# Performance work log

Measured on AMD Instinct MI355X. Metric: run time of the kernel, lower is better.

## Reference

```python
import math
import jax, jax.numpy as jnp
import numpy as np

NUM_HEADS = 32
NUM_KV_HEADS = 8
HEAD_DIM = 128
ROPE_THETA = 10000.0


def rotate_half(x):
    x1, x2 = jnp.split(x, 2, axis=-1)
    return jnp.concatenate((-x2, x1), axis=-1)


def rope_cos_sin(seq_len, dim, dtype):
    pos = jnp.arange(seq_len, dtype=jnp.float32)[:, None]            # [S,1]
    freqs = jnp.exp(-jnp.arange(0, dim, 2, dtype=jnp.float32) * (math.log(ROPE_THETA) / dim))
    ang = pos * freqs                                                # [S,D/2]
    cos = jnp.concatenate([jnp.cos(ang), jnp.cos(ang)], axis=-1)     # [S,D]
    sin = jnp.concatenate([jnp.sin(ang), jnp.sin(ang)], axis=-1)
    # broadcast over heads: [S,1,D]
    return cos[:, None, :].astype(dtype), sin[:, None, :].astype(dtype)


def setup_inputs() -> dict:
    key = jax.random.key(0)
    k1, k2, k3, k4, k5 = jax.random.split(key, 5)
    B, S, Hd = 1, 2048, 4096
    kv_dim = NUM_KV_HEADS * HEAD_DIM
    s = 0.02
    return {
        "hidden_states": jax.random.normal(k1, (B, S, Hd), jnp.float32),
        "Wq": jax.random.normal(k2, (Hd, Hd), jnp.float32) * s,
        "Wk": jax.random.normal(k3, (kv_dim, Hd), jnp.float32) * s,
        "Wv": jax.random.normal(k4, (kv_dim, Hd), jnp.float32) * s,
        "Wo": jax.random.normal(k5, (Hd, Hd), jnp.float32) * s,
    }


def reference(hidden_states, Wq, Wk, Wv, Wo):
    B, S, _ = hidden_states.shape
    H, KV, D = NUM_HEADS, NUM_KV_HEADS, HEAD_DIM
    groups = H // KV

    q = jnp.einsum('bsh,oh->bso', hidden_states, Wq).reshape(B, S, H, D)
    k = jnp.einsum('bsh,oh->bso', hidden_states, Wk).reshape(B, S, KV, D)
    v = jnp.einsum('bsh,oh->bso', hidden_states, Wv).reshape(B, S, KV, D)

    # GQA: repeat_interleave along head dim
    k = jnp.repeat(k, groups, axis=2)   # [B,S,H,D]
    v = jnp.repeat(v, groups, axis=2)

    cos, sin = rope_cos_sin(S, D, hidden_states.dtype)  # [S,1,D]
    q = q * cos + rotate_half(q) * sin
    k = k * cos + rotate_half(k) * sin

    q = q.transpose(0, 2, 1, 3)  # [B,H,S,D]
    k = k.transpose(0, 2, 1, 3)
    v = v.transpose(0, 2, 1, 3)

    scores = jnp.einsum('bhqd,bhkd->bhqk', q, k) / math.sqrt(D)
    causal = jnp.tril(jnp.ones((S, S), dtype=bool))
    scores = jnp.where(causal, scores, jnp.asarray(-1e9, scores.dtype))
    attn = jax.nn.softmax(scores, axis=-1)

    out = jnp.einsum('bhqk,bhkd->bqhd', attn, v).reshape(B, S, H * D)
    return jnp.einsum('bso,ho->bsh', out, Wo)
```

## Files before the change

kernel.cpp:

```cpp
#include <hip/hip_runtime.h>

#define S_LEN 2048
#define HD    4096
#define NH    32
#define NKV   8
#define DH    128
#define NQKV  6144
#define QKV_STRIDE_B (NQKV * 2)

typedef __bf16 bf16_t;
typedef __bf16 bf16x8 __attribute__((ext_vector_type(8)));
typedef float  f32x4  __attribute__((ext_vector_type(4)));
typedef unsigned short ushort8v __attribute__((ext_vector_type(8)));

__device__ inline unsigned short f2bf_bits(float f) {
  unsigned int u = __builtin_bit_cast(unsigned int, f);
  unsigned int r = (u + 0x7FFFu + ((u >> 16) & 1u)) >> 16;
  return (unsigned short)r;
}
__device__ inline bf16_t f2bf(float f) {
  return __builtin_bit_cast(bf16_t, f2bf_bits(f));
}
__device__ inline float bf2f(bf16_t b) {
  unsigned int u = ((unsigned int)__builtin_bit_cast(unsigned short, b)) << 16;
  return __builtin_bit_cast(float, u);
}

__device__ inline void load_lds16(const void* g, void* l) {
  __builtin_amdgcn_global_load_lds(
      (__attribute__((address_space(1))) unsigned int*)(void*)g,
      (__attribute__((address_space(3))) unsigned int*)l, 16, 0, 0);
}

__device__ inline void store_out(float* p, float v)  { *p = v; }
__device__ inline void store_out(bf16_t* p, float v) { *p = f2bf(v); }

__global__ void cvt_all_kernel(const float* __restrict__ s0, const float* __restrict__ s1,
                               const float* __restrict__ s2, const float* __restrict__ s3,
                               const float* __restrict__ s4,
                               long n0, long n1, long n2, long n3,
                               long total, bf16_t* __restrict__ dst) {
  long stride = (long)gridDim.x * blockDim.x;
  for (long i = (long)blockIdx.x * blockDim.x + threadIdx.x; i < total; i += stride) {
    const float* src;
    long rel = i;
    if (rel < n0) src = s0;
    else {
      rel -= n0;
      if (rel < n1) src = s1;
      else {
        rel -= n1;
        if (rel < n2) src = s2;
        else {
          rel -= n2;
          if (rel < n3) src = s3;
          else { rel -= n3; src = s4; }
        }
      }
    }
    float4 v0 = reinterpret_cast<const float4*>(src)[rel * 2];
    float4 v1 = reinterpret_cast<const float4*>(src)[rel * 2 + 1];
    ushort8v o;
    o[0] = f2bf_bits(v0.x); o[1] = f2bf_bits(v0.y);
    o[2] = f2bf_bits(v0.z); o[3] = f2bf_bits(v0.w);
    o[4] = f2bf_bits(v1.x); o[5] = f2bf_bits(v1.y);
    o[6] = f2bf_bits(v1.z); o[7] = f2bf_bits(v1.w);
    reinterpret_cast<ushort8v*>(dst)[i] = o;
  }
}

template <typename OutT>
__global__ __launch_bounds__(256)
void gemm_db32_kernel(const bf16_t* __restrict__ A, const bf16_t* __restrict__ B,
                      OutT* __restrict__ C, int M, int N, int K, int nbx) {
  __shared__ __align__(16) bf16_t lA[2][128 * 32];
  __shared__ __align__(16) bf16_t lB[2][128 * 32];
  const int t = threadIdx.x;
  const int lane = t & 63, wave = t >> 6;

  const int nwg = gridDim.x;
  const int orig = blockIdx.x;
  const int xcd = orig & 7;
  const int qq = nwg >> 3, rr = nwg & 7;
  const int base = (xcd < rr) ? xcd * (qq + 1) : rr * (qq + 1) + (xcd - rr) * qq;
  const int wgid = base + (orig >> 3);
  const int row0 = (wgid / nbx) * 128, col0 = (wgid % nbx) * 128;

  const int wm = (wave >> 1) * 64, wn = (wave & 1) * 64;

  const int rA = wave * 32 + (lane >> 2);
  const int cA = (lane & 3) * 8;
  const char* Asrc0 = (const char*)(A + (size_t)(row0 + rA) * K + cA);
  const char* Asrc1 = (const char*)(A + (size_t)(row0 + rA + 16) * K + cA);
  const char* Bsrc0 = (const char*)(B + (size_t)(col0 + rA) * K + cA);
  const char* Bsrc1 = (const char*)(B + (size_t)(col0 + rA + 16) * K + cA);

  const int fr = lane & 15, fq = lane >> 4;
  f32x4 acc[4][4] = {};

  auto stage = [&](int b, int k0) {
    const size_t kb = (size_t)k0 * 2;
    char* lAd = (char*)lA[b] + wave * 2048;
    char* lBd = (char*)lB[b] + wave * 2048;
    load_lds16(Asrc0 + kb, lAd);
    load_lds16(Asrc1 + kb, lAd + 1024);
    load_lds16(Bsrc0 + kb, lBd);
    load_lds16(Bsrc1 + kb, lBd + 1024);
  };

  stage(0, 0);
  int b = 0;
  for (int k0 = 0; k0 < K; k0 += 32) {
    __syncthreads();
    if (k0 + 32 < K) stage(b ^ 1, k0 + 32);

    bf16x8 af[4], bfv[4];
#pragma unroll
    for (int mi = 0; mi < 4; mi++)
      af[mi] = *reinterpret_cast<const bf16x8*>(&lA[b][(wm + mi * 16 + fr) * 32 + fq * 8]);
#pragma unroll
    for (int ni = 0; ni < 4; ni++)
      bfv[ni] = *reinterpret_cast<const bf16x8*>(&lB[b][(wn + ni * 16 + fr) * 32 + fq * 8]);
    __builtin_amdgcn_s_setprio(1);
#pragma unroll
    for (int mi = 0; mi < 4; mi++)
#pragma unroll
      for (int ni = 0; ni < 4; ni++)
        acc[mi][ni] = __builtin_amdgcn_mfma_f32_16x16x32_bf16(af[mi], bfv[ni], acc[mi][ni], 0, 0, 0);
    __builtin_amdgcn_s_setprio(0);
    b ^= 1;
  }

#pragma unroll
  for (int mi = 0; mi < 4; mi++) {
#pragma unroll
    for (int r = 0; r < 4; r++) {
      int row = row0 + wm + mi * 16 + fq * 4 + r;
      OutT* Cp = C + (size_t)row * N + col0 + wn + fr;
#pragma unroll
      for (int ni = 0; ni < 4; ni++) store_out(Cp + ni * 16, acc[mi][ni][r]);
    }
  }
}

template <typename OutT>
__global__ __launch_bounds__(256)
void gemm_db32_m64_kernel(const bf16_t* __restrict__ A, const bf16_t* __restrict__ B,
                          OutT* __restrict__ C, int M, int N, int K, int nbx) {
  __shared__ __align__(16) bf16_t lA[2][64 * 32];
  __shared__ __align__(16) bf16_t lB[2][128 * 32];
  const int t = threadIdx.x;
  const int lane = t & 63, wave = t >> 6;

  const int nwg = gridDim.x;
  const int orig = blockIdx.x;
  const int xcd = orig & 7;
  const int qq = nwg >> 3, rr = nwg & 7;
  const int base = (xcd < rr) ? xcd * (qq + 1) : rr * (qq + 1) + (xcd - rr) * qq;
  const int wgid = base + (orig >> 3);
  const int row0 = (wgid / nbx) * 64, col0 = (wgid % nbx) * 128;

  const int wm = (wave >> 1) * 32, wn = (wave & 1) * 64;

  const int rA64 = wave * 16 + (lane >> 2);
  const int cA = (lane & 3) * 8;
  const char* Asrc0 = (const char*)(A + (size_t)(row0 + rA64) * K + cA);
  const int rB = wave * 32 + (lane >> 2);
  const char* Bsrc0 = (const char*)(B + (size_t)(col0 + rB) * K + cA);
  const char* Bsrc1 = (const char*)(B + (size_t)(col0 + rB + 16) * K + cA);

  const int fr = lane & 15, fq = lane >> 4;
  f32x4 acc[2][4] = {};

  auto stage = [&](int b, int k0) {
    const size_t kb = (size_t)k0 * 2;
    char* lAd = (char*)lA[b] + wave * 1024;
    char* lBd = (char*)lB[b] + wave * 2048;
    load_lds16(Asrc0 + kb, lAd);
    load_lds16(Bsrc0 + kb, lBd);
    load_lds16(Bsrc1 + kb, lBd + 1024);
  };

  stage(0, 0);
  int b = 0;
  for (int k0 = 0; k0 < K; k0 += 32) {
    __syncthreads();
    if (k0 + 32 < K) stage(b ^ 1, k0 + 32);

    bf16x8 af[2], bfv[4];
#pragma unroll
    for (int mi = 0; mi < 2; mi++)
      af[mi] = *reinterpret_cast<const bf16x8*>(&lA[b][(wm + mi * 16 + fr) * 32 + fq * 8]);
#pragma unroll
    for (int ni = 0; ni < 4; ni++)
      bfv[ni] = *reinterpret_cast<const bf16x8*>(&lB[b][(wn + ni * 16 + fr) * 32 + fq * 8]);
    __builtin_amdgcn_s_setprio(1);
#pragma unroll
    for (int mi = 0; mi < 2; mi++)
#pragma unroll
      for (int ni = 0; ni < 4; ni++)
        acc[mi][ni] = __builtin_amdgcn_mfma_f32_16x16x32_bf16(af[mi], bfv[ni], acc[mi][ni], 0, 0, 0);
    __builtin_amdgcn_s_setprio(0);
    b ^= 1;
  }

#pragma unroll
  for (int mi = 0; mi < 2; mi++) {
#pragma unroll
    for (int r = 0; r < 4; r++) {
      int row = row0 + wm + mi * 16 + fq * 4 + r;
      OutT* Cp = C + (size_t)row * N + col0 + wn + fr;
#pragma unroll
      for (int ni = 0; ni < 4; ni++) store_out(Cp + ni * 16, acc[mi][ni][r]);
    }
  }
}

__global__ void rope_all_kernel(bf16_t* __restrict__ qkv, float qscale) {
  int idx = blockIdx.x * blockDim.x + threadIdx.x;
  int i = idx & 63;
  int hh = (idx >> 6) % (NH + NKV);
  int s = idx / (64 * (NH + NKV));
  const float NEG_LOG1E4_64 = -0.14391156f;
  float freq = __expf((float)i * NEG_LOG1E4_64);
  float ang = (float)s * freq;
  float sn, cs;
  __sincosf(ang, &sn, &cs);
  const int colbase = (hh < NH) ? hh * DH : HD + (hh - NH) * DH;
  const float scale = (hh < NH) ? qscale : 1.0f;
  bf16_t* p = qkv + (size_t)s * NQKV + colbase;
  float x1 = bf2f(p[i]);
  float x2 = bf2f(p[i + 64]);
  p[i]      = f2bf((x1 * cs - x2 * sn) * scale);
  p[i + 64] = f2bf((x2 * cs + x1 * sn) * scale);
}

__global__ void transpose_kernel(const bf16_t* __restrict__ in, bf16_t* __restrict__ out,
                                 int R, int C, int in_rstride) {
  __shared__ bf16_t tile[64][65];
  int c0 = blockIdx.x * 64, r0 = blockIdx.y * 64;
  int t = threadIdx.x;
#pragma unroll
  for (int i = 0; i < 16; i++) {
    int idx = t + i * 256;
    int r = idx >> 6, c = idx & 63;
    tile[r][c] = in[(size_t)(r0 + r) * in_rstride + c0 + c];
  }
  __syncthreads();
#pragma unroll
  for (int i = 0; i < 16; i++) {
    int idx = t + i * 256;
    int r = idx >> 6, c = idx & 63;
    out[(size_t)(c0 + r) * R + r0 + c] = tile[c][r];
  }
}

__global__ __launch_bounds__(256)
void attn_kernel(const bf16_t* __restrict__ Qkv, const bf16_t* __restrict__ Vt,
                 bf16_t* __restrict__ O) {
  __shared__ __align__(16) char lK[2][64 * 256];
  __shared__ __align__(16) char lV[2][64 * 256];
  __shared__ __align__(16) bf16_t lP[4][16 * 72];

  const int t = threadIdx.x, lane = t & 63, wave = t >> 6;
  const int h = blockIdx.y, kvh = h >> 2;
  const int pid = blockIdx.x;
  const int fr = lane & 15, fq = lane >> 4;

  const int gc = wave * 4 + (lane >> 4);
  const int sS = (lane & 15) ^ (gc & 15);
  const char* KsrcB = (const char*)(Qkv + HD + (size_t)kvh * DH) +
                      (size_t)gc * QKV_STRIDE_B + sS * 16;
  const int dVc = gc * 2 + (sS >> 3);
  const char* VsrcB = (const char*)Vt + (size_t)kvh * DH * S_LEN * 2 +
                      (size_t)dVc * 4096 + (sS & 7) * 16;
  char* dKw = (char*)lK[0] + wave * 1024;
  char* dVw = (char*)lV[0] + wave * 1024;

  auto stage = [&](int buf, int kv0) {
    char* dk = dKw + buf * (64 * 256);
    char* dv = dVw + buf * (64 * 256);
    const char* ks = KsrcB + (size_t)kv0 * QKV_STRIDE_B;
    const char* vs = VsrcB + (size_t)kv0 * 2;
#pragma unroll
    for (int i = 0; i < 4; i++) {
      load_lds16(ks + i * (16 * QKV_STRIDE_B), dk + i * 4096);
      load_lds16(vs + i * (size_t)(32 * 4096), dv + i * 4096);
    }
  };

  stage(0, 0);
  int buf = 0;

  for (int pass = 0; pass < 2; pass++) {
    const int qb = pass ? pid : (31 - pid);
    const int q0 = qb * 64 + wave * 16;

    bf16x8 qf[4];
    const bf16_t* Qp = Qkv + (size_t)(q0 + fr) * NQKV + h * DH + fq * 8;
#pragma unroll
    for (int kt = 0; kt < 4; kt++)
      qf[kt] = *reinterpret_cast<const bf16x8*>(Qp + kt * 32);

    f32x4 o_acc[8] = {};
    float m_run[4] = {-1e30f, -1e30f, -1e30f, -1e30f};
    float l_run[4] = {0.f, 0.f, 0.f, 0.f};

    for (int tt = 0; tt <= qb; tt++) {
      __syncthreads();
      if (tt < qb)            stage(buf ^ 1, (tt + 1) * 64);
      else if (pass == 0)     stage(buf ^ 1, 0);

      const char* cK = lK[buf];
      const char* cV = lV[buf];
      const bool diag = (tt == qb);

      f32x4 s_acc[4] = {};
      __builtin_amdgcn_s_setprio(1);
#pragma unroll
      for (int nt = 0; nt < 4; nt++) {
        const char* rowp = cK + (nt * 16 + fr) * 256;
#pragma unroll
        for (int kt = 0; kt < 4; kt++) {
          const bf16x8 kf = *reinterpret_cast<const bf16x8*>(
              rowp + (((kt * 4 + fq) ^ fr) << 4));
          s_acc[nt] = __builtin_amdgcn_mfma_f32_16x16x32_bf16(qf[kt], kf, s_acc[nt], 0, 0, 0);
        }
      }
      __builtin_amdgcn_s_setprio(0);

      float pmax[4];
#pragma unroll
      for (int r = 0; r < 4; r++) {
        if (diag) {
          const int qrel = wave * 16 + fq * 4 + r;
#pragma unroll
          for (int nt = 0; nt < 4; nt++)
            if (nt * 16 + fr > qrel) s_acc[nt][r] = -1e30f;
        }
        float mr = fmaxf(fmaxf(s_acc[0][r], s_acc[1][r]), fmaxf(s_acc[2][r], s_acc[3][r]));
#pragma unroll
        for (int off = 1; off < 16; off <<= 1) mr = fmaxf(mr, __shfl_xor(mr, off, 16));
        pmax[r] = mr;
      }
      bool nb = (pmax[0] > m_run[0] + 8.f) || (pmax[1] > m_run[1] + 8.f) ||
                (pmax[2] > m_run[2] + 8.f) || (pmax[3] > m_run[3] + 8.f);
      if (__any(nb)) {
#pragma unroll
        for (int r = 0; r < 4; r++) {
          float mnew = fmaxf(m_run[r], pmax[r]);
          float alpha = __expf(m_run[r] - mnew);
#pragma unroll
          for (int ni = 0; ni < 8; ni++) o_acc[ni][r] *= alpha;
          l_run[r] *= alpha;
          m_run[r] = mnew;
        }
      }
      bf16_t* lPw = lP[wave];
#pragma unroll
      for (int r = 0; r < 4; r++) {
        float p0 = __expf(s_acc[0][r] - m_run[r]);
        float p1 = __expf(s_acc[1][r] - m_run[r]);
        float p2 = __expf(s_acc[2][r] - m_run[r]);
        float p3 = __expf(s_acc[3][r] - m_run[r]);
        float sr = (p0 + p1) + (p2 + p3);
#pragma unroll
        for (int off = 1; off < 16; off <<= 1) sr += __shfl_xor(sr, off, 16);
        l_run[r] += sr;
        const int row = fq * 4 + r;
        lPw[row * 72 + fr]      = f2bf(p0);
        lPw[row * 72 + 16 + fr] = f2bf(p1);
        lPw[row * 72 + 32 + fr] = f2bf(p2);
        lPw[row * 72 + 48 + fr] = f2bf(p3);
      }

#pragma unroll
      for (int kk = 0; kk < 2; kk++) {
        const bf16x8 pf = *reinterpret_cast<const bf16x8*>(lPw + fr * 72 + kk * 32 + fq * 8);
        __builtin_amdgcn_s_setprio(1);
#pragma unroll
        for (int ni = 0; ni < 8; ni++) {
          const int d = ni * 16 + fr;
          const int g = d >> 1;
          const int slot = ((d & 1) * 8 + kk * 4 + fq) ^ (g & 15);
          const bf16x8 vf = *reinterpret_cast<const bf16x8*>(cV + g * 256 + (slot << 4));
          o_acc[ni] = __builtin_amdgcn_mfma_f32_16x16x32_bf16(pf, vf, o_acc[ni], 0, 0, 0);
        }
        __builtin_amdgcn_s_setprio(0);
      }
      buf ^= 1;
    }

#pragma unroll
    for (int r = 0; r < 4; r++) {
      int qrow = q0 + fq * 4 + r;
      float inv = 1.0f / l_run[r];
      bf16_t* Op = O + ((size_t)qrow * NH + h) * DH + fr;
#pragma unroll
      for (int ni = 0; ni < 8; ni++) Op[ni * 16] = f2bf(o_acc[ni][r] * inv);
    }
  }
}

extern "C" void kernel_launch(void* const* d_in, const int* in_sizes, int n_in,
                              void* d_out, int out_size, void* d_ws, size_t ws_size,
                              hipStream_t stream) {
  const float* X  = (const float*)d_in[0];
  const float* Wq = (const float*)d_in[1];
  const float* Wk = (const float*)d_in[2];
  const float* Wv = (const float*)d_in[3];
  const float* Wo = (const float*)d_in[4];
  float* out = (float*)d_out;

  char* ws = (char*)d_ws;
  size_t off = 0;
  auto alloc = [&](size_t bytes) {
    char* p = ws + off;
    off += (bytes + 255) & ~(size_t)255;
    return p;
  };
  const size_t kvdim = (size_t)NKV * DH;
  bf16_t* Xb    = (bf16_t*)alloc((size_t)S_LEN * HD * 2);
  bf16_t* Wqkvb = (bf16_t*)alloc((size_t)NQKV * HD * 2);
  bf16_t* Wob   = (bf16_t*)alloc((size_t)HD * HD * 2);
  bf16_t* QKVb  = (bf16_t*)alloc((size_t)S_LEN * NQKV * 2);
  bf16_t* Vtb   = (bf16_t*)alloc((size_t)S_LEN * kvdim * 2);
  bf16_t* AOb   = (bf16_t*)alloc((size_t)S_LEN * HD * 2);
  (void)ws_size;

  {
    const long n0 = (long)S_LEN * HD / 8;
    const long n1 = (long)HD * HD / 8;
    const long n2 = (long)kvdim * HD / 8;
    const long n3 = (long)kvdim * HD / 8;
    const long n4 = (long)HD * HD / 8;
    const long total = n0 + n1 + n2 + n3 + n4;
    cvt_all_kernel<<<dim3(2048), dim3(256), 0, stream>>>(
        X, Wq, Wk, Wv, Wo, n0, n1, n2, n3, total, Xb);
  }

  {
    int nbx = NQKV / 128, nby = S_LEN / 128;
    gemm_db32_kernel<bf16_t><<<dim3(nbx * nby), dim3(256), 0, stream>>>(
        Xb, Wqkvb, QKVb, S_LEN, NQKV, HD, nbx);
  }

  rope_all_kernel<<<dim3(S_LEN * (NH + NKV) * 64 / 256), dim3(256), 0, stream>>>(
      QKVb, 0.08838834764831845f);

  transpose_kernel<<<dim3((int)kvdim / 64, S_LEN / 64), dim3(256), 0, stream>>>(
      QKVb + HD + kvdim, Vtb, S_LEN, (int)kvdim, NQKV);

  attn_kernel<<<dim3(16, NH), dim3(256), 0, stream>>>(QKVb, Vtb, AOb);

  {
    int nbx = HD / 128, nby = S_LEN / 64;
    gemm_db32_m64_kernel<float><<<dim3(nbx * nby), dim3(256), 0, stream>>>(
        AOb, Wob, out, S_LEN, HD, HD, nbx);
  }
}
```

Baseline: 361.3 us.

## Fuse fp32-to-bf16 conversion into GEMM tile loads and drop convert kernel

Removes the standalone kernel that converted the input and all weights to bf16. Both GEMMs now read fp32 directly, convert to bf16 in registers and write the tiles to LDS. The QKV GEMM selects Wq, Wk or Wv per column tile. The aim is to eliminate the extra pass over global memory and the kernel launch. The output projection also moves from 64x128 to 128x128 tiles. In exchange, the GEMMs fetch twice the bytes per tile and stage through registers instead of direct global-to-LDS loads, which may raise latency and register pressure.

```diff
diff --git a/kernel.cpp b/kernel.cpp
--- a/kernel.cpp
+++ b/kernel.cpp
@@ -11,7 +11,6 @@
 typedef __bf16 bf16_t;
 typedef __bf16 bf16x8 __attribute__((ext_vector_type(8)));
 typedef float  f32x4  __attribute__((ext_vector_type(4)));
-typedef unsigned short ushort8v __attribute__((ext_vector_type(8)));
 
 __device__ inline unsigned short f2bf_bits(float f) {
   unsigned int u = __builtin_bit_cast(unsigned int, f);
@@ -25,6 +24,12 @@
   unsigned int u = ((unsigned int)__builtin_bit_cast(unsigned short, b)) << 16;
   return __builtin_bit_cast(float, u);
 }
+__device__ inline bf16x8 cvt8(float4 a, float4 b) {
+  bf16x8 o;
+  o[0] = f2bf(a.x); o[1] = f2bf(a.y); o[2] = f2bf(a.z); o[3] = f2bf(a.w);
+  o[4] = f2bf(b.x); o[5] = f2bf(b.y); o[6] = f2bf(b.z); o[7] = f2bf(b.w);
+  return o;
+}
 
 __device__ inline void load_lds16(const void* g, void* l) {
   __builtin_amdgcn_global_load_lds(
@@ -35,44 +40,10 @@
 __device__ inline void store_out(float* p, float v)  { *p = v; }
 __device__ inline void store_out(bf16_t* p, float v) { *p = f2bf(v); }
 
-__global__ void cvt_all_kernel(const float* __restrict__ s0, const float* __restrict__ s1,
-                               const float* __restrict__ s2, const float* __restrict__ s3,
-                               const float* __restrict__ s4,
-                               long n0, long n1, long n2, long n3,
-                               long total, bf16_t* __restrict__ dst) {
-  long stride = (long)gridDim.x * blockDim.x;
-  for (long i = (long)blockIdx.x * blockDim.x + threadIdx.x; i < total; i += stride) {
-    const float* src;
-    long rel = i;
-    if (rel < n0) src = s0;
-    else {
-      rel -= n0;
-      if (rel < n1) src = s1;
-      else {
-        rel -= n1;
-        if (rel < n2) src = s2;
-        else {
-          rel -= n2;
-          if (rel < n3) src = s3;
-          else { rel -= n3; src = s4; }
-        }
-      }
-    }
-    float4 v0 = reinterpret_cast<const float4*>(src)[rel * 2];
-    float4 v1 = reinterpret_cast<const float4*>(src)[rel * 2 + 1];
-    ushort8v o;
-    o[0] = f2bf_bits(v0.x); o[1] = f2bf_bits(v0.y);
-    o[2] = f2bf_bits(v0.z); o[3] = f2bf_bits(v0.w);
-    o[4] = f2bf_bits(v1.x); o[5] = f2bf_bits(v1.y);
-    o[6] = f2bf_bits(v1.z); o[7] = f2bf_bits(v1.w);
-    reinterpret_cast<ushort8v*>(dst)[i] = o;
-  }
-}
-
-template <typename OutT>
 __global__ __launch_bounds__(256)
-void gemm_db32_kernel(const bf16_t* __restrict__ A, const bf16_t* __restrict__ B,
-                      OutT* __restrict__ C, int M, int N, int K, int nbx) {
+void gemm_qkv_kernel(const float* __restrict__ X, const float* __restrict__ Wq,
+                     const float* __restrict__ Wk, const float* __restrict__ Wv,
+                     bf16_t* __restrict__ C, int M, int N, int K, int nbx) {
   __shared__ __align__(16) bf16_t lA[2][128 * 32];
   __shared__ __align__(16) bf16_t lB[2][128 * 32];
   const int t = threadIdx.x;
@@ -88,31 +59,47 @@
 
   const int wm = (wave >> 1) * 64, wn = (wave & 1) * 64;
 
+  const float* Bmat;
+  int bc0;
+  if (col0 < HD)            { Bmat = Wq; bc0 = col0; }
+  else if (col0 < HD + 1024){ Bmat = Wk; bc0 = col0 - HD; }
+  else                      { Bmat = Wv; bc0 = col0 - HD - 1024; }
+
   const int rA = wave * 32 + (lane >> 2);
-  const int cA = (lane & 3) * 8;
-  const char* Asrc0 = (const char*)(A + (size_t)(row0 + rA) * K + cA);
-  const char* Asrc1 = (const char*)(A + (size_t)(row0 + rA + 16) * K + cA);
-  const char* Bsrc0 = (const char*)(B + (size_t)(col0 + rA) * K + cA);
-  const char* Bsrc1 = (const char*)(B + (size_t)(col0 + rA + 16) * K + cA);
+  const int cE = (lane & 3) * 8;
+  const float* As0 = X    + (size_t)(row0 + rA) * K + cE;
+  const float* As1 = X    + (size_t)(row0 + rA + 16) * K + cE;
+  const float* Bs0 = Bmat + (size_t)(bc0 + rA) * K + cE;
+  const float* Bs1 = Bmat + (size_t)(bc0 + rA + 16) * K + cE;
 
   const int fr = lane & 15, fq = lane >> 4;
   f32x4 acc[4][4] = {};
 
-  auto stage = [&](int b, int k0) {
-    const size_t kb = (size_t)k0 * 2;
-    char* lAd = (char*)lA[b] + wave * 2048;
-    char* lBd = (char*)lB[b] + wave * 2048;
-    load_lds16(Asrc0 + kb, lAd);
-    load_lds16(Asrc1 + kb, lAd + 1024);
-    load_lds16(Bsrc0 + kb, lBd);
-    load_lds16(Bsrc1 + kb, lBd + 1024);
+  auto ld4 = [&](const float* p) { return *reinterpret_cast<const float4*>(p); };
+  auto wr = [&](int b, bf16_t* tile, int off, bf16x8 v) {
+    *reinterpret_cast<bf16x8*>((char*)tile + wave * 2048 + off + lane * 16) = v;
   };
 
-  stage(0, 0);
+  {
+    wr(0, lA[0], 0,    cvt8(ld4(As0), ld4(As0 + 4)));
+    wr(0, lA[0], 1024, cvt8(ld4(As1), ld4(As1 + 4)));
+    wr(0, lB[0], 0,    cvt8(ld4(Bs0), ld4(Bs0 + 4)));
+    wr(0, lB[0], 1024, cvt8(ld4(Bs1), ld4(Bs1 + 4)));
+  }
+
   int b = 0;
   for (int k0 = 0; k0 < K; k0 += 32) {
     __syncthreads();
-    if (k0 + 32 < K) stage(b ^ 1, k0 + 32);
+
+    float4 a00, a01, a10, a11, b00, b01, b10, b11;
+    const bool more = (k0 + 32 < K);
+    if (more) {
+      const int e = k0 + 32;
+      a00 = ld4(As0 + e); a01 = ld4(As0 + e + 4);
+      a10 = ld4(As1 + e); a11 = ld4(As1 + e + 4);
+      b00 = ld4(Bs0 + e); b01 = ld4(Bs0 + e + 4);
+      b10 = ld4(Bs1 + e); b11 = ld4(Bs1 + e + 4);
+    }
 
     bf16x8 af[4], bfv[4];
 #pragma unroll
@@ -128,6 +115,13 @@
       for (int ni = 0; ni < 4; ni++)
         acc[mi][ni] = __builtin_amdgcn_mfma_f32_16x16x32_bf16(af[mi], bfv[ni], acc[mi][ni], 0, 0, 0);
     __builtin_amdgcn_s_setprio(0);
+
+    if (more) {
+      wr(b ^ 1, lA[b ^ 1], 0,    cvt8(a00, a01));
+      wr(b ^ 1, lA[b ^ 1], 1024, cvt8(a10, a11));
+      wr(b ^ 1, lB[b ^ 1], 0,    cvt8(b00, b01));
+      wr(b ^ 1, lB[b ^ 1], 1024, cvt8(b10, b11));
+    }
     b ^= 1;
   }
 
@@ -136,18 +130,17 @@
 #pragma unroll
     for (int r = 0; r < 4; r++) {
       int row = row0 + wm + mi * 16 + fq * 4 + r;
-      OutT* Cp = C + (size_t)row * N + col0 + wn + fr;
-#pragma unroll
-      for (int ni = 0; ni < 4; ni++) store_out(Cp + ni * 16, acc[mi][ni][r]);
-    }
-  }
-}
-
-template <typename OutT>
+      bf16_t* Cp = C + (size_t)row * N + col0 + wn + fr;
+#pragma unroll
+      for (int ni = 0; ni < 4; ni++) Cp[ni * 16] = f2bf(acc[mi][ni][r]);
+    }
+  }
+}
+
 __global__ __launch_bounds__(256)
-void gemm_db32_m64_kernel(const bf16_t* __restrict__ A, const bf16_t* __restrict__ B,
-                          OutT* __restrict__ C, int M, int N, int K, int nbx) {
-  __shared__ __align__(16) bf16_t lA[2][64 * 32];
+void gemm_out_kernel(const bf16_t* __restrict__ A, const float* __restrict__ Wo,
+                     float* __restrict__ C, int M, int N, int K, int nbx) {
+  __shared__ __align__(16) bf16_t lA[2][128 * 32];
   __shared__ __align__(16) bf16_t lB[2][128 * 32];
   const int t = threadIdx.x;
   const int lane = t & 63, wave = t >> 6;
@@ -158,60 +151,78 @@
   const int qq = nwg >> 3, rr = nwg & 7;
   const int base = (xcd < rr) ? xcd * (qq + 1) : rr * (qq + 1) + (xcd - rr) * qq;
   const int wgid = base + (orig >> 3);
-  const int row0 = (wgid / nbx) * 64, col0 = (wgid % nbx) * 128;
-
-  const int wm = (wave >> 1) * 32, wn = (wave & 1) * 64;
-
-  const int rA64 = wave * 16 + (lane >> 2);
+  const int row0 = (wgid / nbx) * 128, col0 = (wgid % nbx) * 128;
+
+  const int wm = (wave >> 1) * 64, wn = (wave & 1) * 64;
+
+  const int rA = wave * 32 + (lane >> 2);
   const int cA = (lane & 3) * 8;
-  const char* Asrc0 = (const char*)(A + (size_t)(row0 + rA64) * K + cA);
-  const int rB = wave * 32 + (lane >> 2);
-  const char* Bsrc0 = (const char*)(B + (size_t)(col0 + rB) * K + cA);
-  const char* Bsrc1 = (const char*)(B + (size_t)(col0 + rB + 16) * K + cA);
+  const int cE = (lane & 3) * 8;
+  const char* Asrc0 = (const char*)(A + (size_t)(row0 + rA) * K + cA);
+  const char* Asrc1 = (const char*)(A + (size_t)(row0 + rA + 16) * K + cA);
+  const float* Bs0 = Wo + (size_t)(col0 + rA) * K + cE;
+  const float* Bs1 = Wo + (size_t)(col0 + rA + 16) * K + cE;
 
   const int fr = lane & 15, fq = lane >> 4;
-  f32x4 acc[2][4] = {};
-
-  auto stage = [&](int b, int k0) {
+  f32x4 acc[4][4] = {};
+
+  auto ld4 = [&](const float* p) { return *reinterpret_cast<const float4*>(p); };
+  auto wrB = [&](int b, int off, bf16x8 v) {
+    *reinterpret_cast<bf16x8*>((char*)lB[b] + wave * 2048 + off + lane * 16) = v;
+  };
+  auto stageA = [&](int b, int k0) {
     const size_t kb = (size_t)k0 * 2;
-    char* lAd = (char*)lA[b] + wave * 1024;
-    char* lBd = (char*)lB[b] + wave * 2048;
+    char* lAd = (char*)lA[b] + wave * 2048;
     load_lds16(Asrc0 + kb, lAd);
-    load_lds16(Bsrc0 + kb, lBd);
-    load_lds16(Bsrc1 + kb, lBd + 1024);
+    load_lds16(Asrc1 + kb, lAd + 1024);
   };
 
-  stage(0, 0);
+  stageA(0, 0);
+  wrB(0, 0,    cvt8(ld4(Bs0), ld4(Bs0 + 4)));
+  wrB(0, 1024, cvt8(ld4(Bs1), ld4(Bs1 + 4)));
+
   int b = 0;
   for (int k0 = 0; k0 < K; k0 += 32) {
     __syncthreads();
-    if (k0 + 32 < K) stage(b ^ 1, k0 + 32);
-
-    bf16x8 af[2], bfv[4];
-#pragma unroll
-    for (int mi = 0; mi < 2; mi++)
+    const bool more = (k0 + 32 < K);
+    float4 b00, b01, b10, b11;
+    if (more) {
+      stageA(b ^ 1, k0 + 32);
+      const int e = k0 + 32;
+      b00 = ld4(Bs0 + e); b01 = ld4(Bs0 + e + 4);
+      b10 = ld4(Bs1 + e); b11 = ld4(Bs1 + e + 4);
+    }
+
+    bf16x8 af[4], bfv[4];
+#pragma unroll
+    for (int mi = 0; mi < 4; mi++)
       af[mi] = *reinterpret_cast<const bf16x8*>(&lA[b][(wm + mi * 16 + fr) * 32 + fq * 8]);
 #pragma unroll
     for (int ni = 0; ni < 4; ni++)
       bfv[ni] = *reinterpret_cast<const bf16x8*>(&lB[b][(wn + ni * 16 + fr) * 32 + fq * 8]);
     __builtin_amdgcn_s_setprio(1);
 #pragma unroll
-    for (int mi = 0; mi < 2; mi++)
+    for (int mi = 0; mi < 4; mi++)
 #pragma unroll
       for (int ni = 0; ni < 4; ni++)
         acc[mi][ni] = __builtin_amdgcn_mfma_f32_16x16x32_bf16(af[mi], bfv[ni], acc[mi][ni], 0, 0, 0);
     __builtin_amdgcn_s_setprio(0);
+
+    if (more) {
+      wrB(b ^ 1, 0,    cvt8(b00, b01));
+      wrB(b ^ 1, 1024, cvt8(b10, b11));
+    }
     b ^= 1;
   }
 
 #pragma unroll
-  for (int mi = 0; mi < 2; mi++) {
+  for (int mi = 0; mi < 4; mi++) {
 #pragma unroll
     for (int r = 0; r < 4; r++) {
       int row = row0 + wm + mi * 16 + fq * 4 + r;
-      OutT* Cp = C + (size_t)row * N + col0 + wn + fr;
-#pragma unroll
-      for (int ni = 0; ni < 4; ni++) store_out(Cp + ni * 16, acc[mi][ni][r]);
+      float* Cp = C + (size_t)row * N + col0 + wn + fr;
+#pragma unroll
+      for (int ni = 0; ni < 4; ni++) Cp[ni * 16] = acc[mi][ni][r];
     }
   }
 }
@@ -420,29 +431,15 @@
     return p;
   };
   const size_t kvdim = (size_t)NKV * DH;
-  bf16_t* Xb    = (bf16_t*)alloc((size_t)S_LEN * HD * 2);
-  bf16_t* Wqkvb = (bf16_t*)alloc((size_t)NQKV * HD * 2);
-  bf16_t* Wob   = (bf16_t*)alloc((size_t)HD * HD * 2);
-  bf16_t* QKVb  = (bf16_t*)alloc((size_t)S_LEN * NQKV * 2);
-  bf16_t* Vtb   = (bf16_t*)alloc((size_t)S_LEN * kvdim * 2);
-  bf16_t* AOb   = (bf16_t*)alloc((size_t)S_LEN * HD * 2);
+  bf16_t* QKVb = (bf16_t*)alloc((size_t)S_LEN * NQKV * 2);
+  bf16_t* Vtb  = (bf16_t*)alloc((size_t)S_LEN * kvdim * 2);
+  bf16_t* AOb  = (bf16_t*)alloc((size_t)S_LEN * HD * 2);
   (void)ws_size;
-
-  {
-    const long n0 = (long)S_LEN * HD / 8;
-    const long n1 = (long)HD * HD / 8;
-    const long n2 = (long)kvdim * HD / 8;
-    const long n3 = (long)kvdim * HD / 8;
-    const long n4 = (long)HD * HD / 8;
-    const long total = n0 + n1 + n2 + n3 + n4;
-    cvt_all_kernel<<<dim3(2048), dim3(256), 0, stream>>>(
-        X, Wq, Wk, Wv, Wo, n0, n1, n2, n3, total, Xb);
-  }
 
   {
     int nbx = NQKV / 128, nby = S_LEN / 128;
-    gemm_db32_kernel<bf16_t><<<dim3(nbx * nby), dim3(256), 0, stream>>>(
-        Xb, Wqkvb, QKVb, S_LEN, NQKV, HD, nbx);
+    gemm_qkv_kernel<<<dim3(nbx * nby), dim3(256), 0, stream>>>(
+        X, Wq, Wk, Wv, QKVb, S_LEN, NQKV, HD, nbx);
   }
 
   rope_all_kernel<<<dim3(S_LEN * (NH + NKV) * 64 / 256), dim3(256), 0, stream>>>(
@@ -454,8 +451,8 @@
   attn_kernel<<<dim3(16, NH), dim3(256), 0, stream>>>(QKVb, Vtb, AOb);
 
   {
-    int nbx = HD / 128, nby = S_LEN / 64;
-    gemm_db32_m64_kernel<float><<<dim3(nbx * nby), dim3(256), 0, stream>>>(
-        AOb, Wob, out, S_LEN, HD, HD, nbx);
-  }
-}
+    int nbx = HD / 128, nby = S_LEN / 128;
+    gemm_out_kernel<<<dim3(nbx * nby), dim3(256), 0, stream>>>(
+        AOb, Wo, out, S_LEN, HD, HD, nbx);
+  }
+}
```

Result: slower. 545.0 us (+50.8%).
